# Kernel optimization log

Hardware: AMD Instinct MI355X
Metric: run time of the kernel (lower is better)

The kernel has to match this reference:

```python
import jax, jax.numpy as jnp
import numpy as np

NW, NT, ND = 100000, 20000, 5000      # wallet / token / dev node counts
DW, DT, DD = 32, 32, 16               # raw feature dims
H = 64                                 # GATConv out channels (heads=1)
E_WW, E_BU, E_SE, E_CR = 1600000, 1000000, 1000000, 20000


def setup_inputs() -> dict:
    key = jax.random.key(0)
    ks = iter(jax.random.split(key, 80))

    def nrm(shape, s=1.0):
        return jax.random.normal(next(ks), shape, dtype=jnp.float32) * s

    inp = {
        "x_wallet": nrm((NW, DW)),
        "x_token": nrm((NT, DT)),
        "x_dev": nrm((ND, DD)),
    }
    # per-relation GATConv params: lin_src, lin_dst (bias=False), att_src, att_dst, bias
    rels = [("g1ww", DW, DW), ("g1bu", DW, DT), ("g1se", DW, DT), ("g1cr", DD, DT),
            ("g2ww", H, H), ("g2bu", H, H), ("g2se", H, H)]
    for pre, ds, dd in rels:
        inp[pre + "_Ws"] = nrm((ds, H), 0.1)
        inp[pre + "_Wd"] = nrm((dd, H), 0.1)
        inp[pre + "_as"] = nrm((H,), 0.1)
        inp[pre + "_ad"] = nrm((H,), 0.1)
        inp[pre + "_b"] = nrm((H,), 0.1)
    inp["Wfc"] = nrm((H, 2), 0.1)
    inp["bfc"] = nrm((2,), 0.1)

    for name, n, hi in [("ww_src", E_WW, NW), ("ww_dst", E_WW, NW),
                        ("bu_src", E_BU, NW), ("bu_dst", E_BU, NT),
                        ("se_src", E_SE, NW), ("se_dst", E_SE, NT),
                        ("cr_src", E_CR, ND), ("cr_dst", E_CR, NT)]:
        inp[name] = jax.random.randint(next(ks), (n,), 0, hi, dtype=jnp.int32)
    return inp


def gat(xs, xd, src, dst, Ws, Wd, a_s, a_d, b, n_dst):
    """PyG GATConv, heads=1, add_self_loops=False, negative_slope=0.2."""
    hs = xs @ Ws                                   # [Ns, H]
    e = jax.nn.leaky_relu((hs @ a_s)[src] + ((xd @ Wd) @ a_d)[dst], 0.2)  # [E]
    m = jax.ops.segment_max(e, dst, num_segments=n_dst)
    ex = jnp.exp(e - m[dst])
    den = jax.ops.segment_sum(ex, dst, num_segments=n_dst)
    alpha = ex / (den[dst] + 1e-16)                # scatter-softmax over dst
    out = jax.ops.segment_sum(alpha[:, None] * hs[src], dst, num_segments=n_dst)
    return out + b


def reference(x_wallet, x_token, x_dev,
              g1ww_Ws, g1ww_Wd, g1ww_as, g1ww_ad, g1ww_b,
              g1bu_Ws, g1bu_Wd, g1bu_as, g1bu_ad, g1bu_b,
              g1se_Ws, g1se_Wd, g1se_as, g1se_ad, g1se_b,
              g1cr_Ws, g1cr_Wd, g1cr_as, g1cr_ad, g1cr_b,
              g2ww_Ws, g2ww_Wd, g2ww_as, g2ww_ad, g2ww_b,
              g2bu_Ws, g2bu_Wd, g2bu_as, g2bu_ad, g2bu_b,
              g2se_Ws, g2se_Wd, g2se_as, g2se_ad, g2se_b,
              Wfc, bfc,
              ww_src, ww_dst, bu_src, bu_dst, se_src, se_dst, cr_src, cr_dst):
    # conv1 (HeteroConv, aggr='sum'): dev has no incoming edges -> dropped
    w1 = gat(x_wallet, x_wallet, ww_src, ww_dst, g1ww_Ws, g1ww_Wd, g1ww_as, g1ww_ad, g1ww_b, NW)
    t1 = (gat(x_wallet, x_token, bu_src, bu_dst, g1bu_Ws, g1bu_Wd, g1bu_as, g1bu_ad, g1bu_b, NT)
          + gat(x_wallet, x_token, se_src, se_dst, g1se_Ws, g1se_Wd, g1se_as, g1se_ad, g1se_b, NT)
          + gat(x_dev, x_token, cr_src, cr_dst, g1cr_Ws, g1cr_Wd, g1cr_as, g1cr_ad, g1cr_b, NT))
    # conv2: 'dev' absent from x_dict, so ('dev','creates','token') is skipped by HeteroConv
    w2 = gat(w1, w1, ww_src, ww_dst, g2ww_Ws, g2ww_Wd, g2ww_as, g2ww_ad, g2ww_b, NW)  # computed but unused downstream (matches torch)
    t2 = (gat(w1, t1, bu_src, bu_dst, g2bu_Ws, g2bu_Wd, g2bu_as, g2bu_ad, g2bu_b, NT)
          + gat(w1, t1, se_src, se_dst, g2se_Ws, g2se_Wd, g2se_as, g2se_ad, g2se_b, NT))
    del w2
    return t2 @ Wfc + bfc  # [NT, 2]
```

## Files before the change

kernel.cpp:

```cpp
#include <hip/hip_runtime.h>

#define NW 100000
#define NT 20000
#define ND 5000
#define EWW 1600000
#define EBU 1000000
#define ESE 1000000
#define ECR 20000
#define EPB 16384
#define BBTH 1024
#define SITER 16
#define ABTH 512

#define WWSH 8
#define WWW 256
#define NBWB 391
#define WCAP 6144
#define WITER 12
#define TSH 6
#define TW 64
#define NBTB 313
#define TCAP 4096
#define TITER 8
#define CCAP 512
#define CITER 1

typedef unsigned int uint;

#define R_EDWW 0
#define R_EDBU 1
#define R_EDSE 2
#define R_EDCR 3
#define R_WV2BU 4
#define R_WV2SE 5
#define R_ESWW 6
#define R_ESBU 7
#define R_ESSE 8
#define R_ESCR 9
#define R_WS2BU 10
#define R_WS2SE 11
#define R_VBU 12
#define R_VSE 13
#define R_DBU_B 14
#define R_DSE_B 15
#define R_DBU_S 16
#define R_DSE_S 17
#define R_DBU_C 18
#define R_DSE_C 19
#define R_TBU0 20
#define R_TBU1 21
#define R_TSE0 22
#define R_TSE1 23
#define R_CBU 24
#define R_CSE 25
#define R_SBU 26
#define R_SSE 27
#define R_MBU0 28
#define R_MBU1 29
#define R_MSE0 30
#define R_MSE1 31
#define R_CB1U0 32
#define R_CB1U1 33
#define R_CB1S0 34
#define R_CB1S1 35
#define R_C20 36
#define R_C21 37
#define R_F0 38
#define R_F1 39
#define R_BT1 40
#define R_BT2 41
#define NROWS 42

struct WvN { const float* M[16]; const float* v[16]; int K[16]; };


struct Init1 {
    WvN A;
    const float* Wfc;
    const float* b1a; const float* b1b; const float* b1c;
    const float* b2a; const float* b2b;
    int* ccur;
    float* wvbuf;
};

__global__ __launch_bounds__(256) void k_init1(Init1 a) {
    int bi = blockIdx.x, t = threadIdx.x;
    if (bi < 16) {
        int i = bi * 256 + t;
        int li = i >> 10, j = i & 1023;
        int cap = (li == 0) ? WCAP : (li == 3 ? CCAP : TCAP);
        a.ccur[i] = j * cap;
    } else if (bi == 16) {
        if (t < 64) {
            a.wvbuf[R_F0 * 64 + t] = a.Wfc[t * 2];
            a.wvbuf[R_F1 * 64 + t] = a.Wfc[t * 2 + 1];
        }
    } else if (bi == 17) {
        if (t < 64) a.wvbuf[R_BT1 * 64 + t] = a.b1a[t] + a.b1b[t] + a.b1c[t];
    } else if (bi == 18) {
        if (t < 64) a.wvbuf[R_BT2 * 64 + t] = a.b2a[t] + a.b2b[t];
    } else {
        int b = bi - 19;
        if (t < a.A.K[b]) {
            const float* M = a.A.M[b];
            const float* v = a.A.v[b];
            float s = 0.f;
            for (int j = 0; j < 64; ++j) s = fmaf(M[t * 64 + j], v[j], s);
            a.wvbuf[b * 64 + t] = s;
        }
    }
}


__global__ __launch_bounds__(64) void k_wvN(WvN a, float* __restrict__ out) {
    int b = blockIdx.x, t = threadIdx.x;
    if (t < a.K[b]) {
        const float* M = a.M[b];
        const float* v = a.v[b];
        float s = 0.f;
        for (int j = 0; j < 64; ++j) s = fmaf(M[t * 64 + j], v[j], s);
        out[b * 64 + t] = s;
    }
}


struct BMeta {
    const int* src[4]; const int* dst[4];
    int* ccur[4];
    uint* pairs[4];
    int E[4]; int shift[4]; int cap[4]; int bbase[5];
};

struct Build {
    BMeta bm;
    const float* Xw;
    const float* vw[14];
    float* edww; float* PW; float4* TBt; float4* TSt;
    const float* Xt; const float* Xd;
    const float* tv0; const float* tv1; const float* tv2;
    const float* dv0; const float* dv1; const float* dv2;
    float* e0; float* e1; float* e2;
    float4* TC;
    int nbScat, nbPW, nbPT;
};

__device__ __forceinline__ int find_list(const int* bbase, int b) {
    int li = 0;
    while (li < 3 && b >= bbase[li + 1]) ++li;
    return li;
}

__global__ __launch_bounds__(BBTH) void k_build(Build a) {
    int t = threadIdx.x;
    if ((int)blockIdx.x < a.nbScat) {
        __shared__ int scnt[1024];
        __shared__ int sbase[1024];
        for (int i = t; i < 1024; i += BBTH) scnt[i] = 0;
        __syncthreads();
        int li = find_list(a.bm.bbase, blockIdx.x);
        int lb = blockIdx.x - a.bm.bbase[li];
        const int* src = a.bm.src[li];
        const int* dst = a.bm.dst[li];
        uint* pairs = a.bm.pairs[li];
        int* ccur = a.bm.ccur[li];
        int sh = a.bm.shift[li];
        int cap = a.bm.cap[li];
        uint mask = (1u << sh) - 1u;
        int b0 = lb * EPB;
        int end = min(b0 + EPB, a.bm.E[li]);
        uint pk[SITER];
        int bk[SITER];
        int rk[SITER];
#pragma unroll
        for (int k = 0; k < SITER; ++k) {
            int i = b0 + t + k * BBTH;
            bool v = i < end;
            int d = v ? dst[i] : 0;
            int s = v ? src[i] : 0;
            int b = d >> sh;
            pk[k] = (uint)s | (((uint)d & mask) << 20);
            rk[k] = v ? atomicAdd(&scnt[b], 1) : 0;
            bk[k] = v ? b : -1;
        }
        __syncthreads();
        for (int i = t; i < 1024; i += BBTH) {
            int c = scnt[i];
            sbase[i] = c ? atomicAdd(&ccur[i], c) : 0;
        }
        __syncthreads();
#pragma unroll
        for (int k = 0; k < SITER; ++k) {
            if (bk[k] >= 0) {
                int p = sbase[bk[k]] + rk[k];
                if (p < (bk[k] + 1) * cap)
                    pairs[p] = pk[k];
            }
        }
    } else if ((int)blockIdx.x < a.nbScat + a.nbPW) {
        int bid = blockIdx.x - a.nbScat;
        int wvid = (bid * BBTH + t) >> 6;
        int half = (t >> 5) & 1;
        int l = t & 31;
        int r = wvid * 2 + half;
        float x = (r < NW) ? a.Xw[(size_t)r * 32 + l] : 0.f;
        float p[14];
#pragma unroll
        for (int i = 0; i < 14; ++i) p[i] = x * a.vw[i][l];
#pragma unroll
        for (int o = 1; o < 32; o <<= 1) {
#pragma unroll
            for (int i = 0; i < 14; ++i) p[i] += __shfl_xor(p[i], o, 64);
        }
        if (l == 0 && r < NW) {
            a.edww[r] = p[3];
            float4* P = (float4*)(a.PW + (size_t)r * 8);
            P[0] = make_float4(p[4], p[5], p[6], p[7]);
            P[1] = make_float4(p[8], p[9], p[0], 0.f);
            a.TBt[r] = make_float4(p[10], p[11], p[1], 0.f);
            a.TSt[r] = make_float4(p[12], p[13], p[2], 0.f);
        }
    } else if ((int)blockIdx.x < a.nbScat + a.nbPW + a.nbPT) {
        int bid = blockIdx.x - a.nbScat - a.nbPW;
        int wvid = (bid * BBTH + t) >> 6;
        int half = (t >> 5) & 1;
        int l = t & 31;
        int r = wvid * 2 + half;
        float x = (r < NT) ? a.Xt[(size_t)r * 32 + l] : 0.f;
        float p0 = x * a.tv0[l], p1 = x * a.tv1[l], p2 = x * a.tv2[l];
#pragma unroll
        for (int o = 1; o < 32; o <<= 1) {
            p0 += __shfl_xor(p0, o, 64);
            p1 += __shfl_xor(p1, o, 64);
            p2 += __shfl_xor(p2, o, 64);
        }
        if (l == 0 && r < NT) { a.e0[r] = p0; a.e1[r] = p1; a.e2[r] = p2; }
    } else {
        int bid = blockIdx.x - a.nbScat - a.nbPW - a.nbPT;
        int r = (bid * BBTH + t) >> 4;
        int l = t & 15;
        float x = (r < ND) ? a.Xd[(size_t)r * 16 + l] : 0.f;
        float p0 = x * a.dv0[l], p1 = x * a.dv1[l], p2 = x * a.dv2[l];
#pragma unroll
        for (int o = 1; o < 16; o <<= 1) {
            p0 += __shfl_xor(p0, o, 64);
            p1 += __shfl_xor(p1, o, 64);
            p2 += __shfl_xor(p2, o, 64);
        }
        if (l == 0 && r < ND) a.TC[r] = make_float4(p1, p2, p0, 0.f);
    }
}


template <int ITER>
__device__ __forceinline__ void sort_bucket(const uint* __restrict__ slab, int cnt,
                                            int ndl, uint* sp, int* hoff, int* hcnt,
                                            int t) {
    if (t < ndl) hcnt[t] = 0;
    __syncthreads();
    uint pk[ITER];
    int gk[ITER];
    int rk[ITER];
#pragma unroll
    for (int k = 0; k < ITER; ++k) {
        int i = t + k * ABTH;
        bool v = i < cnt;
        uint pr = v ? slab[i] : 0;
        int g = pr >> 20;
        pk[k] = pr & 0xFFFFFu;
        rk[k] = v ? atomicAdd(&hcnt[g], 1) : 0;
        gk[k] = v ? g : -1;
    }
    __syncthreads();
    int own = (t < ndl) ? hcnt[t] : 0;
    if (t < ndl) hoff[t] = own;
    __syncthreads();
    for (int o = 1; o < ndl; o <<= 1) {
        int u = 0;
        if (t < ndl && t >= o) u = hoff[t - o];
        __syncthreads();
        if (t < ndl && t >= o) hoff[t] += u;
        __syncthreads();
    }
    if (t < ndl) hoff[t] -= own;
    __syncthreads();
#pragma unroll
    for (int k = 0; k < ITER; ++k)
        if (gk[k] >= 0) sp[hoff[gk[k]] + rk[k]] = pk[k];
    __syncthreads();
}


__global__ __launch_bounds__(ABTH) void k_fsaggw(const uint* __restrict__ pairs,
                                                 const int* __restrict__ ccur,
                                                 const float* __restrict__ ed,
                                                 const float* __restrict__ PW,
                                                 const float* __restrict__ C,
                                                 float4* __restrict__ TL2B,
                                                 float4* __restrict__ TL2S) {
    __shared__ uint sp[WCAP];
    __shared__ int hoff[WWW];
    __shared__ int hcnt[WWW];
    __shared__ float eds[WWW];
    int t = threadIdx.x, b = blockIdx.x;
    int d0 = b << WWSH;
    if (t < WWW) {
        int d = d0 + t;
        eds[t] = (d < NW) ? ed[d] : 0.f;
    }
    int cnt = min(ccur[b] - b * WCAP, WCAP);
    sort_bucket<WITER>(pairs + (size_t)b * WCAP, cnt, WWW, sp, hoff, hcnt, t);
    int dl = t >> 1, sub = t & 1;
    float edj = eds[dl];
    float A0 = 0, A1 = 0, A2 = 0, A3 = 0, A4 = 0, A5 = 0, den = 0;
    int s0 = hoff[dl], s1 = s0 + hcnt[dl];
    for (int j = s0 + sub; j < s1; j += 2) {
        int s = sp[j];
        const float4* P = (const float4*)(PW + (size_t)s * 8);
        float4 u = P[0], v = P[1];
        float e = v.z + edj;
        e = e > 0.f ? e : 0.2f * e;
        float w = __expf(e);
        den += w;
        A0 = fmaf(w, u.x, A0); A1 = fmaf(w, u.y, A1); A2 = fmaf(w, u.z, A2);
        A3 = fmaf(w, u.w, A3); A4 = fmaf(w, v.x, A4); A5 = fmaf(w, v.y, A5);
    }
    A0 += __shfl_xor(A0, 1, 64); A1 += __shfl_xor(A1, 1, 64);
    A2 += __shfl_xor(A2, 1, 64); A3 += __shfl_xor(A3, 1, 64);
    A4 += __shfl_xor(A4, 1, 64); A5 += __shfl_xor(A5, 1, 64);
    den += __shfl_xor(den, 1, 64);
    if (sub == 0) {
        int d = d0 + dl;
        if (d < NW) {
            float c0 = C[R_CBU * 64], c1 = C[R_CSE * 64];
            float c2 = C[R_CB1U0 * 64], c3 = C[R_CB1U1 * 64];
            float c4 = C[R_CB1S0 * 64], c5 = C[R_CB1S1 * 64];
            if (den > 0.f) {
                float inv = 1.f / (den + 1e-16f);
                TL2B[d] = make_float4(A2 * inv + c2, A3 * inv + c3, A0 * inv + c0, 0.f);
                TL2S[d] = make_float4(A4 * inv + c4, A5 * inv + c5, A1 * inv + c1, 0.f);
            } else {
                TL2B[d] = make_float4(c2, c3, c0, 0.f);
                TL2S[d] = make_float4(c4, c5, c1, 0.f);
            }
        }
    }
}


__global__ __launch_bounds__(ABTH) void k_fsaggt(const uint* __restrict__ pB,
                                                 const uint* __restrict__ pS,
                                                 const uint* __restrict__ pC,
                                                 const int* __restrict__ curB,
                                                 const int* __restrict__ curS,
                                                 const int* __restrict__ curC,
                                                 const float* __restrict__ edB,
                                                 const float* __restrict__ edS,
                                                 const float* __restrict__ edC,
                                                 const float4* __restrict__ TB,
                                                 const float4* __restrict__ TS,
                                                 const float4* __restrict__ TC,
                                                 const float4* __restrict__ TL2B,
                                                 const float4* __restrict__ TL2S,
                                                 const float* __restrict__ C,
                                                 const float* __restrict__ bfc,
                                                 float* __restrict__ out) {
    __shared__ uint spB[TCAP];
    __shared__ uint spS[TCAP];
    __shared__ uint spC[CCAP];
    __shared__ int hoB[TW], hcB[TW], hoS[TW], hcS[TW], hoC[TW], hcC[TW];
    __shared__ float eds[3][TW];
    int t = threadIdx.x, b = blockIdx.x;
    int d0 = b << TSH;
    if (t < TW) {
        int d = d0 + t;
        eds[0][t] = (d < NT) ? edB[d] : 0.f;
        eds[1][t] = (d < NT) ? edS[d] : 0.f;
        eds[2][t] = (d < NT) ? edC[d] : 0.f;
    }
    int cntB = min(curB[b] - b * TCAP, TCAP);
    int cntS = min(curS[b] - b * TCAP, TCAP);
    int cntC = min(curC[b] - b * CCAP, CCAP);
    sort_bucket<TITER>(pB + (size_t)b * TCAP, cntB, TW, spB, hoB, hcB, t);
    sort_bucket<TITER>(pS + (size_t)b * TCAP, cntS, TW, spS, hoS, hcS, t);
    sort_bucket<CITER>(pC + (size_t)b * CCAP, cntC, TW, spC, hoC, hcC, t);

    int dl = t >> 3, sub = t & 7;

    float bx = 0, by = 0, bd = 0;
    for (int j = hoB[dl] + sub; j < hoB[dl] + hcB[dl]; j += 8) {
        float4 q = TB[spB[j]];
        float e = q.z + eds[0][dl];
        e = e > 0.f ? e : 0.2f * e;
        float w = __expf(e);
        bd += w; bx = fmaf(w, q.x, bx); by = fmaf(w, q.y, by);
    }
    float sx = 0, sy = 0, sd = 0;
    for (int j = hoS[dl] + sub; j < hoS[dl] + hcS[dl]; j += 8) {
        float4 q = TS[spS[j]];
        float e = q.z + eds[1][dl];
        e = e > 0.f ? e : 0.2f * e;
        float w = __expf(e);
        sd += w; sx = fmaf(w, q.x, sx); sy = fmaf(w, q.y, sy);
    }
    float cx = 0, cy = 0, cd = 0;
    for (int j = hoC[dl] + sub; j < hoC[dl] + hcC[dl]; j += 8) {
        float4 q = TC[spC[j]];
        float e = q.z + eds[2][dl];
        e = e > 0.f ? e : 0.2f * e;
        float w = __expf(e);
        cd += w; cx = fmaf(w, q.x, cx); cy = fmaf(w, q.y, cy);
    }
#pragma unroll
    for (int o = 1; o < 8; o <<= 1) {
        bx += __shfl_xor(bx, o, 64); by += __shfl_xor(by, o, 64); bd += __shfl_xor(bd, o, 64);
        sx += __shfl_xor(sx, o, 64); sy += __shfl_xor(sy, o, 64); sd += __shfl_xor(sd, o, 64);
        cx += __shfl_xor(cx, o, 64); cy += __shfl_xor(cy, o, 64); cd += __shfl_xor(cd, o, 64);
    }
    float qbx = 0, qby = 0, qsx = 0, qsy = 0, qcx = 0, qcy = 0;
    if (bd > 0.f) { float i = 1.f / (bd + 1e-16f); qbx = bx * i; qby = by * i; }
    if (sd > 0.f) { float i = 1.f / (sd + 1e-16f); qsx = sx * i; qsy = sy * i; }
    if (cd > 0.f) { float i = 1.f / (cd + 1e-16f); qcx = cx * i; qcy = cy * i; }
    float ed2b = C[R_SBU * 64] + qbx + qsx + qcx;
    float ed2s = C[R_SSE * 64] + qby + qsy + qcy;

    float rbx = 0, rby = 0, rbd = 0;
    for (int j = hoB[dl] + sub; j < hoB[dl] + hcB[dl]; j += 8) {
        float4 q = TL2B[spB[j]];
        float e = q.z + ed2b;
        e = e > 0.f ? e : 0.2f * e;
        float w = __expf(e);
        rbd += w; rbx = fmaf(w, q.x, rbx); rby = fmaf(w, q.y, rby);
    }
    float rsx = 0, rsy = 0, rsd = 0;
    for (int j = hoS[dl] + sub; j < hoS[dl] + hcS[dl]; j += 8) {
        float4 q = TL2S[spS[j]];
        float e = q.z + ed2s;
        e = e > 0.f ? e : 0.2f * e;
        float w = __expf(e);
        rsd += w; rsx = fmaf(w, q.x, rsx); rsy = fmaf(w, q.y, rsy);
    }
#pragma unroll
    for (int o = 1; o < 8; o <<= 1) {
        rbx += __shfl_xor(rbx, o, 64); rby += __shfl_xor(rby, o, 64); rbd += __shfl_xor(rbd, o, 64);
        rsx += __shfl_xor(rsx, o, 64); rsy += __shfl_xor(rsy, o, 64); rsd += __shfl_xor(rsd, o, 64);
    }
    if (sub == 0) {
        int d = d0 + dl;
        if (d < NT) {
            float fbx = 0, fby = 0, fsx = 0, fsy = 0;
            if (rbd > 0.f) { float i = 1.f / (rbd + 1e-16f); fbx = rbx * i; fby = rby * i; }
            if (rsd > 0.f) { float i = 1.f / (rsd + 1e-16f); fsx = rsx * i; fsy = rsy * i; }
            out[d * 2 + 0] = bfc[0] + C[R_C20 * 64] + fbx + fsx;
            out[d * 2 + 1] = bfc[1] + C[R_C21 * 64] + fby + fsy;
        }
    }
}


extern "C" void kernel_launch(void* const* d_in, const int* in_sizes, int n_in,
                              void* d_out, int out_size, void* d_ws, size_t ws_size,
                              hipStream_t stream) {
    const float* xw = (const float*)d_in[0];
    const float* xt = (const float*)d_in[1];
    const float* xd = (const float*)d_in[2];
    const float* g1ww_Ws = (const float*)d_in[3];
    const float* g1ww_Wd = (const float*)d_in[4];
    const float* g1ww_as = (const float*)d_in[5];
    const float* g1ww_ad = (const float*)d_in[6];
    const float* g1ww_b  = (const float*)d_in[7];
    const float* g1bu_Ws = (const float*)d_in[8];
    const float* g1bu_Wd = (const float*)d_in[9];
    const float* g1bu_as = (const float*)d_in[10];
    const float* g1bu_ad = (const float*)d_in[11];
    const float* g1bu_b  = (const float*)d_in[12];
    const float* g1se_Ws = (const float*)d_in[13];
    const float* g1se_Wd = (const float*)d_in[14];
    const float* g1se_as = (const float*)d_in[15];
    const float* g1se_ad = (const float*)d_in[16];
    const float* g1se_b  = (const float*)d_in[17];
    const float* g1cr_Ws = (const float*)d_in[18];
    const float* g1cr_Wd = (const float*)d_in[19];
    const float* g1cr_as = (const float*)d_in[20];
    const float* g1cr_ad = (const float*)d_in[21];
    const float* g1cr_b  = (const float*)d_in[22];
    const float* g2bu_Ws = (const float*)d_in[28];
    const float* g2bu_Wd = (const float*)d_in[29];
    const float* g2bu_as = (const float*)d_in[30];
    const float* g2bu_ad = (const float*)d_in[31];
    const float* g2bu_b  = (const float*)d_in[32];
    const float* g2se_Ws = (const float*)d_in[33];
    const float* g2se_Wd = (const float*)d_in[34];
    const float* g2se_as = (const float*)d_in[35];
    const float* g2se_ad = (const float*)d_in[36];
    const float* g2se_b  = (const float*)d_in[37];
    const float* Wfc = (const float*)d_in[38];
    const float* bfc = (const float*)d_in[39];
    const int* ww_src = (const int*)d_in[40];
    const int* ww_dst = (const int*)d_in[41];
    const int* bu_src = (const int*)d_in[42];
    const int* bu_dst = (const int*)d_in[43];
    const int* se_src = (const int*)d_in[44];
    const int* se_dst = (const int*)d_in[45];
    const int* cr_src = (const int*)d_in[46];
    const int* cr_dst = (const int*)d_in[47];

    char* p = (char*)d_ws;
    auto alloc = [&](size_t bytes) {
        char* r = p;
        p += (bytes + 255) & ~(size_t)255;
        return r;
    };
    uint* pairsW = (uint*)alloc((size_t)NBWB * WCAP * 4);
    uint* pairsB = (uint*)alloc((size_t)NBTB * TCAP * 4);
    uint* pairsS = (uint*)alloc((size_t)NBTB * TCAP * 4);
    uint* pairsC = (uint*)alloc((size_t)NBTB * CCAP * 4);
    int* ccur = (int*)alloc(4 * 1024 * 4);

    float* wvbuf = (float*)alloc(NROWS * 64 * 4);

    float* edww = (float*)alloc((size_t)NW * 4);
    float* edbu = (float*)alloc((size_t)NT * 4);
    float* edse = (float*)alloc((size_t)NT * 4);
    float* edcr = (float*)alloc((size_t)NT * 4);
    float* PW   = (float*)alloc((size_t)NW * 8 * 4);
    float4* TB  = (float4*)alloc((size_t)NW * 16);
    float4* TS  = (float4*)alloc((size_t)NW * 16);
    float4* TC  = (float4*)alloc((size_t)ND * 16);
    float4* TL2B = (float4*)alloc((size_t)NW * 16);
    float4* TL2S = (float4*)alloc((size_t)NW * 16);

    const int nbW_e = (EWW + EPB - 1) / EPB;
    const int nbB_e = (EBU + EPB - 1) / EPB;
    const int nbS_e = (ESE + EPB - 1) / EPB;
    const int nbC_e = (ECR + EPB - 1) / EPB;
    const int nbScat = nbW_e + nbB_e + nbS_e + nbC_e;
    const int nbPW = (NW + 31) / 32;
    const int nbPT = (NT + 31) / 32;
    const int nbPD = (ND + 63) / 64;

    Init1 i1;
    i1.A.M[0] = g1ww_Wd; i1.A.v[0] = g1ww_ad; i1.A.K[0] = 32;
    i1.A.M[1] = g1bu_Wd; i1.A.v[1] = g1bu_ad; i1.A.K[1] = 32;
    i1.A.M[2] = g1se_Wd; i1.A.v[2] = g1se_ad; i1.A.K[2] = 32;
    i1.A.M[3] = g1cr_Wd; i1.A.v[3] = g1cr_ad; i1.A.K[3] = 32;
    i1.A.M[4] = g2bu_Wd; i1.A.v[4] = g2bu_ad; i1.A.K[4] = 64;
    i1.A.M[5] = g2se_Wd; i1.A.v[5] = g2se_ad; i1.A.K[5] = 64;
    i1.A.M[6] = g1ww_Ws; i1.A.v[6] = g1ww_as; i1.A.K[6] = 32;
    i1.A.M[7] = g1bu_Ws; i1.A.v[7] = g1bu_as; i1.A.K[7] = 32;
    i1.A.M[8] = g1se_Ws; i1.A.v[8] = g1se_as; i1.A.K[8] = 32;
    i1.A.M[9] = g1cr_Ws; i1.A.v[9] = g1cr_as; i1.A.K[9] = 16;
    i1.A.M[10] = g2bu_Ws; i1.A.v[10] = g2bu_as; i1.A.K[10] = 64;
    i1.A.M[11] = g2se_Ws; i1.A.v[11] = g2se_as; i1.A.K[11] = 64;
    for (int i = 12; i < 16; ++i) { i1.A.M[i] = nullptr; i1.A.v[i] = nullptr; i1.A.K[i] = 0; }
    i1.Wfc = Wfc;
    i1.b1a = g1bu_b; i1.b1b = g1se_b; i1.b1c = g1cr_b;
    i1.b2a = g2bu_b; i1.b2b = g2se_b;
    i1.ccur = ccur;
    i1.wvbuf = wvbuf;
    k_init1<<<31, 256, 0, stream>>>(i1);

    WvN B;
    B.M[0] = g1ww_Ws; B.v[0] = wvbuf + R_WS2BU * 64; B.K[0] = 32;
    B.M[1] = g1ww_Ws; B.v[1] = wvbuf + R_WS2SE * 64; B.K[1] = 32;
    B.M[2] = g1bu_Ws; B.v[2] = wvbuf + R_WV2BU * 64; B.K[2] = 32;
    B.M[3] = g1bu_Ws; B.v[3] = wvbuf + R_WV2SE * 64; B.K[3] = 32;
    B.M[4] = g1se_Ws; B.v[4] = wvbuf + R_WV2BU * 64; B.K[4] = 32;
    B.M[5] = g1se_Ws; B.v[5] = wvbuf + R_WV2SE * 64; B.K[5] = 32;
    B.M[6] = g1cr_Ws; B.v[6] = wvbuf + R_WV2BU * 64; B.K[6] = 16;
    B.M[7] = g1cr_Ws; B.v[7] = wvbuf + R_WV2SE * 64; B.K[7] = 16;
    B.M[8] = g2bu_Ws; B.v[8] = wvbuf + R_F0 * 64; B.K[8] = 64;
    B.M[9] = g2bu_Ws; B.v[9] = wvbuf + R_F1 * 64; B.K[9] = 64;
    B.M[10] = g2se_Ws; B.v[10] = wvbuf + R_F0 * 64; B.K[10] = 64;
    B.M[11] = g2se_Ws; B.v[11] = wvbuf + R_F1 * 64; B.K[11] = 64;
    B.M[12] = g1ww_b; B.v[12] = wvbuf + R_WS2BU * 64; B.K[12] = 1;
    B.M[13] = g1ww_b; B.v[13] = wvbuf + R_WS2SE * 64; B.K[13] = 1;
    B.M[14] = wvbuf + R_BT1 * 64; B.v[14] = wvbuf + R_WV2BU * 64; B.K[14] = 1;
    B.M[15] = wvbuf + R_BT1 * 64; B.v[15] = wvbuf + R_WV2SE * 64; B.K[15] = 1;
    k_wvN<<<16, 64, 0, stream>>>(B, wvbuf + R_VBU * 64);

    WvN Cc;
    Cc.M[0] = g1ww_Ws; Cc.v[0] = wvbuf + R_TBU0 * 64; Cc.K[0] = 32;
    Cc.M[1] = g1ww_Ws; Cc.v[1] = wvbuf + R_TBU1 * 64; Cc.K[1] = 32;
    Cc.M[2] = g1ww_Ws; Cc.v[2] = wvbuf + R_TSE0 * 64; Cc.K[2] = 32;
    Cc.M[3] = g1ww_Ws; Cc.v[3] = wvbuf + R_TSE1 * 64; Cc.K[3] = 32;
    Cc.M[4] = g1ww_b; Cc.v[4] = wvbuf + R_TBU0 * 64; Cc.K[4] = 1;
    Cc.M[5] = g1ww_b; Cc.v[5] = wvbuf + R_TBU1 * 64; Cc.K[5] = 1;
    Cc.M[6] = g1ww_b; Cc.v[6] = wvbuf + R_TSE0 * 64; Cc.K[6] = 1;
    Cc.M[7] = g1ww_b; Cc.v[7] = wvbuf + R_TSE1 * 64; Cc.K[7] = 1;
    Cc.M[8] = wvbuf + R_BT2 * 64; Cc.v[8] = wvbuf + R_F0 * 64; Cc.K[8] = 1;
    Cc.M[9] = wvbuf + R_BT2 * 64; Cc.v[9] = wvbuf + R_F1 * 64; Cc.K[9] = 1;
    for (int i = 10; i < 16; ++i) { Cc.M[i] = nullptr; Cc.v[i] = nullptr; Cc.K[i] = 0; }
    k_wvN<<<10, 64, 0, stream>>>(Cc, wvbuf + R_MBU0 * 64);

    Build bd;
    bd.bm.src[0] = ww_src; bd.bm.dst[0] = ww_dst; bd.bm.ccur[0] = ccur + 0 * 1024;
    bd.bm.pairs[0] = pairsW; bd.bm.E[0] = EWW; bd.bm.shift[0] = WWSH; bd.bm.cap[0] = WCAP;
    bd.bm.src[1] = bu_src; bd.bm.dst[1] = bu_dst; bd.bm.ccur[1] = ccur + 1 * 1024;
    bd.bm.pairs[1] = pairsB; bd.bm.E[1] = EBU; bd.bm.shift[1] = TSH; bd.bm.cap[1] = TCAP;
    bd.bm.src[2] = se_src; bd.bm.dst[2] = se_dst; bd.bm.ccur[2] = ccur + 2 * 1024;
    bd.bm.pairs[2] = pairsS; bd.bm.E[2] = ESE; bd.bm.shift[2] = TSH; bd.bm.cap[2] = TCAP;
    bd.bm.src[3] = cr_src; bd.bm.dst[3] = cr_dst; bd.bm.ccur[3] = ccur + 3 * 1024;
    bd.bm.pairs[3] = pairsC; bd.bm.E[3] = ECR; bd.bm.shift[3] = TSH; bd.bm.cap[3] = CCAP;
    bd.bm.bbase[0] = 0; bd.bm.bbase[1] = nbW_e; bd.bm.bbase[2] = nbW_e + nbB_e;
    bd.bm.bbase[3] = nbW_e + nbB_e + nbS_e; bd.bm.bbase[4] = nbScat;
    bd.Xw = xw;
    bd.vw[0] = wvbuf + R_ESWW * 64; bd.vw[1] = wvbuf + R_ESBU * 64;
    bd.vw[2] = wvbuf + R_ESSE * 64; bd.vw[3] = wvbuf + R_EDWW * 64;
    bd.vw[4] = wvbuf + R_VBU * 64;  bd.vw[5] = wvbuf + R_VSE * 64;
    bd.vw[6] = wvbuf + R_MBU0 * 64; bd.vw[7] = wvbuf + R_MBU1 * 64;
    bd.vw[8] = wvbuf + R_MSE0 * 64; bd.vw[9] = wvbuf + R_MSE1 * 64;
    bd.vw[10] = wvbuf + R_DBU_B * 64; bd.vw[11] = wvbuf + R_DSE_B * 64;
    bd.vw[12] = wvbuf + R_DBU_S * 64; bd.vw[13] = wvbuf + R_DSE_S * 64;
    bd.edww = edww; bd.PW = PW; bd.TBt = TB; bd.TSt = TS;
    bd.Xt = xt; bd.Xd = xd;
    bd.tv0 = wvbuf + R_EDBU * 64; bd.tv1 = wvbuf + R_EDSE * 64; bd.tv2 = wvbuf + R_EDCR * 64;
    bd.dv0 = wvbuf + R_ESCR * 64; bd.dv1 = wvbuf + R_DBU_C * 64; bd.dv2 = wvbuf + R_DSE_C * 64;
    bd.e0 = edbu; bd.e1 = edse; bd.e2 = edcr;
    bd.TC = TC;
    bd.nbScat = nbScat; bd.nbPW = nbPW; bd.nbPT = nbPT;
    k_build<<<nbScat + nbPW + nbPT + nbPD, BBTH, 0, stream>>>(bd);

    k_fsaggw<<<NBWB, ABTH, 0, stream>>>(pairsW, ccur + 0 * 1024, edww, PW, wvbuf,
                                        TL2B, TL2S);

    k_fsaggt<<<NBTB, ABTH, 0, stream>>>(pairsB, pairsS, pairsC,
                                        ccur + 1 * 1024, ccur + 2 * 1024, ccur + 3 * 1024,
                                        edbu, edse, edcr,
                                        TB, TS, TC, TL2B, TL2S,
                                        wvbuf, bfc, (float*)d_out);
}
```

Before: 273.6 us.

## Merge wallet and token layer-1 aggregation into one launch, split token layer-2

```diff
diff --git a/kernel.cpp b/kernel.cpp
--- a/kernel.cpp
+++ b/kernel.cpp
@@ -290,141 +290,185 @@
 }
 
 
-__global__ __launch_bounds__(ABTH) void k_fsaggw(const uint* __restrict__ pairs,
-                                                 const int* __restrict__ ccur,
-                                                 const float* __restrict__ ed,
-                                                 const float* __restrict__ PW,
-                                                 const float* __restrict__ C,
-                                                 float4* __restrict__ TL2B,
-                                                 float4* __restrict__ TL2S) {
-    __shared__ uint sp[WCAP];
-    __shared__ int hoff[WWW];
-    __shared__ int hcnt[WWW];
-    __shared__ float eds[WWW];
-    int t = threadIdx.x, b = blockIdx.x;
-    int d0 = b << WWSH;
-    if (t < WWW) {
-        int d = d0 + t;
-        eds[t] = (d < NW) ? ed[d] : 0.f;
-    }
-    int cnt = min(ccur[b] - b * WCAP, WCAP);
-    sort_bucket<WITER>(pairs + (size_t)b * WCAP, cnt, WWW, sp, hoff, hcnt, t);
-    int dl = t >> 1, sub = t & 1;
-    float edj = eds[dl];
-    float A0 = 0, A1 = 0, A2 = 0, A3 = 0, A4 = 0, A5 = 0, den = 0;
-    int s0 = hoff[dl], s1 = s0 + hcnt[dl];
-    for (int j = s0 + sub; j < s1; j += 2) {
-        int s = sp[j];
-        const float4* P = (const float4*)(PW + (size_t)s * 8);
-        float4 u = P[0], v = P[1];
-        float e = v.z + edj;
-        e = e > 0.f ? e : 0.2f * e;
-        float w = __expf(e);
-        den += w;
-        A0 = fmaf(w, u.x, A0); A1 = fmaf(w, u.y, A1); A2 = fmaf(w, u.z, A2);
-        A3 = fmaf(w, u.w, A3); A4 = fmaf(w, v.x, A4); A5 = fmaf(w, v.y, A5);
-    }
-    A0 += __shfl_xor(A0, 1, 64); A1 += __shfl_xor(A1, 1, 64);
-    A2 += __shfl_xor(A2, 1, 64); A3 += __shfl_xor(A3, 1, 64);
-    A4 += __shfl_xor(A4, 1, 64); A5 += __shfl_xor(A5, 1, 64);
-    den += __shfl_xor(den, 1, 64);
-    if (sub == 0) {
-        int d = d0 + dl;
-        if (d < NW) {
-            float c0 = C[R_CBU * 64], c1 = C[R_CSE * 64];
-            float c2 = C[R_CB1U0 * 64], c3 = C[R_CB1U1 * 64];
-            float c4 = C[R_CB1S0 * 64], c5 = C[R_CB1S1 * 64];
-            if (den > 0.f) {
-                float inv = 1.f / (den + 1e-16f);
-                TL2B[d] = make_float4(A2 * inv + c2, A3 * inv + c3, A0 * inv + c0, 0.f);
-                TL2S[d] = make_float4(A4 * inv + c4, A5 * inv + c5, A1 * inv + c1, 0.f);
-            } else {
-                TL2B[d] = make_float4(c2, c3, c0, 0.f);
-                TL2S[d] = make_float4(c4, c5, c1, 0.f);
+union SMem1 {
+    struct {
+        uint sp[WCAP];
+        int hoff[WWW]; int hcnt[WWW];
+        float eds[WWW];
+    } w;
+    struct {
+        uint spB[TCAP]; uint spS[TCAP]; uint spC[CCAP];
+        int hoB[TW], hcB[TW], hoS[TW], hcS[TW], hoC[TW], hcC[TW];
+        float eds[3][TW];
+    } tk;
+};
+
+__global__ __launch_bounds__(ABTH) void k_fsagg1(
+        uint* __restrict__ pairsW, uint* __restrict__ pB,
+        uint* __restrict__ pS, const uint* __restrict__ pC,
+        const int* __restrict__ curW, const int* __restrict__ curB,
+        const int* __restrict__ curS, const int* __restrict__ curC,
+        const float* __restrict__ edWW, const float* __restrict__ edB,
+        const float* __restrict__ edS, const float* __restrict__ edC,
+        const float* __restrict__ PW,
+        const float4* __restrict__ TB, const float4* __restrict__ TS,
+        const float4* __restrict__ TC,
+        const float* __restrict__ C,
+        float4* __restrict__ TL2B, float4* __restrict__ TL2S,
+        float* __restrict__ ed2bu, float* __restrict__ ed2se,
+        int* __restrict__ hoBg, int* __restrict__ hoSg) {
+    __shared__ SMem1 sm;
+    int t = threadIdx.x;
+    if ((int)blockIdx.x < NBWB) {
+        int b = blockIdx.x;
+        int d0 = b << WWSH;
+        if (t < WWW) {
+            int d = d0 + t;
+            sm.w.eds[t] = (d < NW) ? edWW[d] : 0.f;
+        }
+        int cnt = min(curW[b] - b * WCAP, WCAP);
+        sort_bucket<WITER>(pairsW + (size_t)b * WCAP, cnt, WWW, sm.w.sp, sm.w.hoff, sm.w.hcnt, t);
+        int dl = t >> 1, sub = t & 1;
+        float edj = sm.w.eds[dl];
+        float A0 = 0, A1 = 0, A2 = 0, A3 = 0, A4 = 0, A5 = 0, den = 0;
+        int s0 = sm.w.hoff[dl], s1 = s0 + sm.w.hcnt[dl];
+        for (int j = s0 + sub; j < s1; j += 2) {
+            int s = sm.w.sp[j];
+            const float4* P = (const float4*)(PW + (size_t)s * 8);
+            float4 u = P[0], v = P[1];
+            float e = v.z + edj;
+            e = e > 0.f ? e : 0.2f * e;
+            float w = __expf(e);
+            den += w;
+            A0 = fmaf(w, u.x, A0); A1 = fmaf(w, u.y, A1); A2 = fmaf(w, u.z, A2);
+            A3 = fmaf(w, u.w, A3); A4 = fmaf(w, v.x, A4); A5 = fmaf(w, v.y, A5);
+        }
+        A0 += __shfl_xor(A0, 1, 64); A1 += __shfl_xor(A1, 1, 64);
+        A2 += __shfl_xor(A2, 1, 64); A3 += __shfl_xor(A3, 1, 64);
+        A4 += __shfl_xor(A4, 1, 64); A5 += __shfl_xor(A5, 1, 64);
+        den += __shfl_xor(den, 1, 64);
+        if (sub == 0) {
+            int d = d0 + dl;
+            if (d < NW) {
+                float c0 = C[R_CBU * 64], c1 = C[R_CSE * 64];
+                float c2 = C[R_CB1U0 * 64], c3 = C[R_CB1U1 * 64];
+                float c4 = C[R_CB1S0 * 64], c5 = C[R_CB1S1 * 64];
+                if (den > 0.f) {
+                    float inv = 1.f / (den + 1e-16f);
+                    TL2B[d] = make_float4(A2 * inv + c2, A3 * inv + c3, A0 * inv + c0, 0.f);
+                    TL2S[d] = make_float4(A4 * inv + c4, A5 * inv + c5, A1 * inv + c1, 0.f);
+                } else {
+                    TL2B[d] = make_float4(c2, c3, c0, 0.f);
+                    TL2S[d] = make_float4(c4, c5, c1, 0.f);
+                }
             }
         }
-    }
-}
-
-
-__global__ __launch_bounds__(ABTH) void k_fsaggt(const uint* __restrict__ pB,
-                                                 const uint* __restrict__ pS,
-                                                 const uint* __restrict__ pC,
-                                                 const int* __restrict__ curB,
-                                                 const int* __restrict__ curS,
-                                                 const int* __restrict__ curC,
-                                                 const float* __restrict__ edB,
-                                                 const float* __restrict__ edS,
-                                                 const float* __restrict__ edC,
-                                                 const float4* __restrict__ TB,
-                                                 const float4* __restrict__ TS,
-                                                 const float4* __restrict__ TC,
-                                                 const float4* __restrict__ TL2B,
-                                                 const float4* __restrict__ TL2S,
-                                                 const float* __restrict__ C,
-                                                 const float* __restrict__ bfc,
-                                                 float* __restrict__ out) {
+    } else {
+        int b = blockIdx.x - NBWB;
+        int d0 = b << TSH;
+        if (t < TW) {
+            int d = d0 + t;
+            sm.tk.eds[0][t] = (d < NT) ? edB[d] : 0.f;
+            sm.tk.eds[1][t] = (d < NT) ? edS[d] : 0.f;
+            sm.tk.eds[2][t] = (d < NT) ? edC[d] : 0.f;
+        }
+        int cntB = min(curB[b] - b * TCAP, TCAP);
+        int cntS = min(curS[b] - b * TCAP, TCAP);
+        int cntC = min(curC[b] - b * CCAP, CCAP);
+        sort_bucket<TITER>(pB + (size_t)b * TCAP, cntB, TW, sm.tk.spB, sm.tk.hoB, sm.tk.hcB, t);
+        sort_bucket<TITER>(pS + (size_t)b * TCAP, cntS, TW, sm.tk.spS, sm.tk.hoS, sm.tk.hcS, t);
+        sort_bucket<CITER>(pC + (size_t)b * CCAP, cntC, TW, sm.tk.spC, sm.tk.hoC, sm.tk.hcC, t);
+
+        int dl = t >> 3, sub = t & 7;
+
+        float bx = 0, by = 0, bd = 0;
+        for (int j = sm.tk.hoB[dl] + sub; j < sm.tk.hoB[dl] + sm.tk.hcB[dl]; j += 8) {
+            float4 q = TB[sm.tk.spB[j]];
+            float e = q.z + sm.tk.eds[0][dl];
+            e = e > 0.f ? e : 0.2f * e;
+            float w = __expf(e);
+            bd += w; bx = fmaf(w, q.x, bx); by = fmaf(w, q.y, by);
+        }
+        float sx = 0, sy = 0, sd = 0;
+        for (int j = sm.tk.hoS[dl] + sub; j < sm.tk.hoS[dl] + sm.tk.hcS[dl]; j += 8) {
+            float4 q = TS[sm.tk.spS[j]];
+            float e = q.z + sm.tk.eds[1][dl];
+            e = e > 0.f ? e : 0.2f * e;
+            float w = __expf(e);
+            sd += w; sx = fmaf(w, q.x, sx); sy = fmaf(w, q.y, sy);
+        }
+        float cx = 0, cy = 0, cd = 0;
+        for (int j = sm.tk.hoC[dl] + sub; j < sm.tk.hoC[dl] + sm.tk.hcC[dl]; j += 8) {
+            float4 q = TC[sm.tk.spC[j]];
+            float e = q.z + sm.tk.eds[2][dl];
+            e = e > 0.f ? e : 0.2f * e;
+            float w = __expf(e);
+            cd += w; cx = fmaf(w, q.x, cx); cy = fmaf(w, q.y, cy);
+        }
+#pragma unroll
+        for (int o = 1; o < 8; o <<= 1) {
+            bx += __shfl_xor(bx, o, 64); by += __shfl_xor(by, o, 64); bd += __shfl_xor(bd, o, 64);
+            sx += __shfl_xor(sx, o, 64); sy += __shfl_xor(sy, o, 64); sd += __shfl_xor(sd, o, 64);
+            cx += __shfl_xor(cx, o, 64); cy += __shfl_xor(cy, o, 64); cd += __shfl_xor(cd, o, 64);
+        }
+        if (sub == 0) {
+            int d = d0 + dl;
+            if (d < NT) {
+                float qbx = 0, qby = 0, qsx = 0, qsy = 0, qcx = 0, qcy = 0;
+                if (bd > 0.f) { float i = 1.f / (bd + 1e-16f); qbx = bx * i; qby = by * i; }
+                if (sd > 0.f) { float i = 1.f / (sd + 1e-16f); qsx = sx * i; qsy = sy * i; }
+                if (cd > 0.f) { float i = 1.f / (cd + 1e-16f); qcx = cx * i; qcy = cy * i; }
+                ed2bu[d] = C[R_SBU * 64] + qbx + qsx + qcx;
+                ed2se[d] = C[R_SSE * 64] + qby + qsy + qcy;
+            }
+        }
+        for (int i = t; i < cntB; i += ABTH) pB[(size_t)b * TCAP + i] = sm.tk.spB[i];
+        for (int i = t; i < cntS; i += ABTH) pS[(size_t)b * TCAP + i] = sm.tk.spS[i];
+        if (t < TW) {
+            hoBg[b * 65 + t] = sm.tk.hoB[t];
+            hoSg[b * 65 + t] = sm.tk.hoS[t];
+        }
+        if (t == 0) {
+            hoBg[b * 65 + 64] = cntB;
+            hoSg[b * 65 + 64] = cntS;
+        }
+    }
+}
+
+
+__global__ __launch_bounds__(ABTH) void k_fsagg2(
+        const uint* __restrict__ pB, const uint* __restrict__ pS,
+        const int* __restrict__ hoBg, const int* __restrict__ hoSg,
+        const float* __restrict__ ed2bu, const float* __restrict__ ed2se,
+        const float4* __restrict__ TL2B, const float4* __restrict__ TL2S,
+        const float* __restrict__ C, const float* __restrict__ bfc,
+        float* __restrict__ out) {
     __shared__ uint spB[TCAP];
     __shared__ uint spS[TCAP];
-    __shared__ uint spC[CCAP];
-    __shared__ int hoB[TW], hcB[TW], hoS[TW], hcS[TW], hoC[TW], hcC[TW];
-    __shared__ float eds[3][TW];
+    __shared__ int hoB[65], hoS[65];
+    __shared__ float edsB[TW], edsS[TW];
     int t = threadIdx.x, b = blockIdx.x;
     int d0 = b << TSH;
+    if (t < 65) {
+        hoB[t] = hoBg[b * 65 + t];
+        hoS[t] = hoSg[b * 65 + t];
+    }
     if (t < TW) {
         int d = d0 + t;
-        eds[0][t] = (d < NT) ? edB[d] : 0.f;
-        eds[1][t] = (d < NT) ? edS[d] : 0.f;
-        eds[2][t] = (d < NT) ? edC[d] : 0.f;
-    }
-    int cntB = min(curB[b] - b * TCAP, TCAP);
-    int cntS = min(curS[b] - b * TCAP, TCAP);
-    int cntC = min(curC[b] - b * CCAP, CCAP);
-    sort_bucket<TITER>(pB + (size_t)b * TCAP, cntB, TW, spB, hoB, hcB, t);
-    sort_bucket<TITER>(pS + (size_t)b * TCAP, cntS, TW, spS, hoS, hcS, t);
-    sort_bucket<CITER>(pC + (size_t)b * CCAP, cntC, TW, spC, hoC, hcC, t);
-
+        edsB[t] = (d < NT) ? ed2bu[d] : 0.f;
+        edsS[t] = (d < NT) ? ed2se[d] : 0.f;
+    }
+    __syncthreads();
+    int cntB = hoB[64], cntS = hoS[64];
+    for (int i = t; i < cntB; i += ABTH) spB[i] = pB[(size_t)b * TCAP + i];
+    for (int i = t; i < cntS; i += ABTH) spS[i] = pS[(size_t)b * TCAP + i];
+    __syncthreads();
     int dl = t >> 3, sub = t & 7;
-
-    float bx = 0, by = 0, bd = 0;
-    for (int j = hoB[dl] + sub; j < hoB[dl] + hcB[dl]; j += 8) {
-        float4 q = TB[spB[j]];
-        float e = q.z + eds[0][dl];
-        e = e > 0.f ? e : 0.2f * e;
-        float w = __expf(e);
-        bd += w; bx = fmaf(w, q.x, bx); by = fmaf(w, q.y, by);
-    }
-    float sx = 0, sy = 0, sd = 0;
-    for (int j = hoS[dl] + sub; j < hoS[dl] + hcS[dl]; j += 8) {
-        float4 q = TS[spS[j]];
-        float e = q.z + eds[1][dl];
-        e = e > 0.f ? e : 0.2f * e;
-        float w = __expf(e);
-        sd += w; sx = fmaf(w, q.x, sx); sy = fmaf(w, q.y, sy);
-    }
-    float cx = 0, cy = 0, cd = 0;
-    for (int j = hoC[dl] + sub; j < hoC[dl] + hcC[dl]; j += 8) {
-        float4 q = TC[spC[j]];
-        float e = q.z + eds[2][dl];
-        e = e > 0.f ? e : 0.2f * e;
-        float w = __expf(e);
-        cd += w; cx = fmaf(w, q.x, cx); cy = fmaf(w, q.y, cy);
-    }
-#pragma unroll
-    for (int o = 1; o < 8; o <<= 1) {
-        bx += __shfl_xor(bx, o, 64); by += __shfl_xor(by, o, 64); bd += __shfl_xor(bd, o, 64);
-        sx += __shfl_xor(sx, o, 64); sy += __shfl_xor(sy, o, 64); sd += __shfl_xor(sd, o, 64);
-        cx += __shfl_xor(cx, o, 64); cy += __shfl_xor(cy, o, 64); cd += __shfl_xor(cd, o, 64);
-    }
-    float qbx = 0, qby = 0, qsx = 0, qsy = 0, qcx = 0, qcy = 0;
-    if (bd > 0.f) { float i = 1.f / (bd + 1e-16f); qbx = bx * i; qby = by * i; }
-    if (sd > 0.f) { float i = 1.f / (sd + 1e-16f); qsx = sx * i; qsy = sy * i; }
-    if (cd > 0.f) { float i = 1.f / (cd + 1e-16f); qcx = cx * i; qcy = cy * i; }
-    float ed2b = C[R_SBU * 64] + qbx + qsx + qcx;
-    float ed2s = C[R_SSE * 64] + qby + qsy + qcy;
-
+    int sB0 = hoB[dl], sB1 = (dl < TW - 1) ? hoB[dl + 1] : cntB;
+    int sS0 = hoS[dl], sS1 = (dl < TW - 1) ? hoS[dl + 1] : cntS;
+    float ed2b = edsB[dl], ed2s = edsS[dl];
     float rbx = 0, rby = 0, rbd = 0;
-    for (int j = hoB[dl] + sub; j < hoB[dl] + hcB[dl]; j += 8) {
+    for (int j = sB0 + sub; j < sB1; j += 8) {
         float4 q = TL2B[spB[j]];
         float e = q.z + ed2b;
         e = e > 0.f ? e : 0.2f * e;
@@ -432,7 +476,7 @@
         rbd += w; rbx = fmaf(w, q.x, rbx); rby = fmaf(w, q.y, rby);
     }
     float rsx = 0, rsy = 0, rsd = 0;
-    for (int j = hoS[dl] + sub; j < hoS[dl] + hcS[dl]; j += 8) {
+    for (int j = sS0 + sub; j < sS1; j += 8) {
         float4 q = TL2S[spS[j]];
         float e = q.z + ed2s;
         e = e > 0.f ? e : 0.2f * e;
@@ -522,12 +566,16 @@
     float* edbu = (float*)alloc((size_t)NT * 4);
     float* edse = (float*)alloc((size_t)NT * 4);
     float* edcr = (float*)alloc((size_t)NT * 4);
+    float* ed2bu = (float*)alloc((size_t)NT * 4);
+    float* ed2se = (float*)alloc((size_t)NT * 4);
     float* PW   = (float*)alloc((size_t)NW * 8 * 4);
     float4* TB  = (float4*)alloc((size_t)NW * 16);
     float4* TS  = (float4*)alloc((size_t)NW * 16);
     float4* TC  = (float4*)alloc((size_t)ND * 16);
     float4* TL2B = (float4*)alloc((size_t)NW * 16);
     float4* TL2S = (float4*)alloc((size_t)NW * 16);
+    int* hoBg = (int*)alloc((size_t)NBTB * 65 * 4);
+    int* hoSg = (int*)alloc((size_t)NBTB * 65 * 4);
 
     const int nbW_e = (EWW + EPB - 1) / EPB;
     const int nbB_e = (EBU + EPB - 1) / EPB;
@@ -620,12 +668,14 @@
     bd.nbScat = nbScat; bd.nbPW = nbPW; bd.nbPT = nbPT;
     k_build<<<nbScat + nbPW + nbPT + nbPD, BBTH, 0, stream>>>(bd);
 
-    k_fsaggw<<<NBWB, ABTH, 0, stream>>>(pairsW, ccur + 0 * 1024, edww, PW, wvbuf,
-                                        TL2B, TL2S);
-
-    k_fsaggt<<<NBTB, ABTH, 0, stream>>>(pairsB, pairsS, pairsC,
-                                        ccur + 1 * 1024, ccur + 2 * 1024, ccur + 3 * 1024,
-                                        edbu, edse, edcr,
-                                        TB, TS, TC, TL2B, TL2S,
-                                        wvbuf, bfc, (float*)d_out);
-}
+    k_fsagg1<<<NBWB + NBTB, ABTH, 0, stream>>>(
+        pairsW, pairsB, pairsS, pairsC,
+        ccur + 0 * 1024, ccur + 1 * 1024, ccur + 2 * 1024, ccur + 3 * 1024,
+        edww, edbu, edse, edcr,
+        PW, TB, TS, TC, wvbuf,
+        TL2B, TL2S, ed2bu, ed2se, hoBg, hoSg);
+
+    k_fsagg2<<<NBTB, ABTH, 0, stream>>>(
+        pairsB, pairsS, hoBg, hoSg, ed2bu, ed2se,
+        TL2B, TL2S, wvbuf, bfc, (float*)d_out);
+}
```

New measurement: 268.8 us. Within noise of the previous version (-1.7%).
